# Performance work log

Measured on AMD Instinct MI355X. Metric: run time of the kernel, lower is better.

## Reference

```python
import jax, jax.numpy as jnp
import numpy as np

D_MODEL = 1024
D_FEATURE = 64
N_HEADS = D_MODEL // D_FEATURE  # 16


def setup_inputs() -> dict:
    key = jax.random.key(0)
    ks = jax.random.split(key, 11)
    B, S = 2, 2048
    s = 1.0 / np.sqrt(D_MODEL)
    inp = {
        "queries": jax.random.normal(ks[0], (B, S, D_MODEL), dtype=jnp.float32),
        "keys": jax.random.normal(ks[1], (B, S, D_MODEL), dtype=jnp.float32),
        "values": jax.random.normal(ks[2], (B, S, D_MODEL), dtype=jnp.float32),
        # Per-head Q/K/V projection weights stacked over heads: [H, d_model, d_feature]
        "Wq": jax.random.normal(ks[3], (N_HEADS, D_MODEL, D_FEATURE), dtype=jnp.float32) * s,
        "Wk": jax.random.normal(ks[4], (N_HEADS, D_MODEL, D_FEATURE), dtype=jnp.float32) * s,
        "Wv": jax.random.normal(ks[5], (N_HEADS, D_MODEL, D_FEATURE), dtype=jnp.float32) * s,
        "bq": jax.random.normal(ks[6], (N_HEADS, D_FEATURE), dtype=jnp.float32) * 0.01,
        "bk": jax.random.normal(ks[7], (N_HEADS, D_FEATURE), dtype=jnp.float32) * 0.01,
        "bv": jax.random.normal(ks[8], (N_HEADS, D_FEATURE), dtype=jnp.float32) * 0.01,
        # Output projection Linear(d_model, d_model)
        "Wo": jax.random.normal(ks[9], (D_MODEL, D_MODEL), dtype=jnp.float32) * s,
        "bo": jax.random.normal(ks[10], (D_MODEL,), dtype=jnp.float32) * 0.01,
    }
    return inp


def reference(queries, keys, values, Wq, Wk, Wv, bq, bk, bv, Wo, bo):
    # Batched equivalent of the per-head loop: all heads' Q/K/V projections
    # done as single einsums, fused multi-head scaled-dot-product attention,
    # then concat (reshape) + output projection. Dropout is identity (eval).
    scale = 1.0 / jnp.sqrt(jnp.asarray(D_FEATURE, queries.dtype))
    q = jnp.einsum("bsd,hdf->bhsf", queries, Wq) + bq[None, :, None, :]
    k = jnp.einsum("bsd,hdf->bhsf", keys, Wk) + bk[None, :, None, :]
    v = jnp.einsum("bsd,hdf->bhsf", values, Wv) + bv[None, :, None, :]
    scores = jnp.einsum("bhsf,bhtf->bhst", q, k) * scale  # [B,H,S,S]
    attn = jax.nn.softmax(scores, axis=-1)
    out = jnp.einsum("bhst,bhtf->bhsf", attn, v)  # [B,H,S,F]
    B, H, S, F = out.shape
    # torch.cat(heads, dim=2): head outputs laid out contiguously -> (h f)
    out = out.transpose(0, 2, 1, 3).reshape(B, S, H * F)
    return out @ Wo.T + bo  # final Linear(d_model, d_model)
```

## Files before the change

kernel.cpp:

```cpp
#include <hip/hip_runtime.h>
#include <hip/hip_bf16.h>

typedef __bf16 bf16_t;
typedef __bf16 bf16x4 __attribute__((ext_vector_type(4)));
typedef __bf16 bf16x8 __attribute__((ext_vector_type(8)));
typedef _Float16 f16_t;
typedef _Float16 f16x4 __attribute__((ext_vector_type(4)));
typedef _Float16 f16x8 __attribute__((ext_vector_type(8)));
typedef float f32x4 __attribute__((ext_vector_type(4)));

#define MFMA16(a, b, c)  __builtin_amdgcn_mfma_f32_16x16x32_bf16((a), (b), (c), 0, 0, 0)
#define MFMA16H(a, b, c) __builtin_amdgcn_mfma_f32_16x16x16f16((a), (b), (c), 0, 0, 0)

#define QSCALE 0.18033688089869237f

typedef __attribute__((address_space(3))) void lds_void;
typedef const __attribute__((address_space(1))) void glob_void;
static __device__ __forceinline__ void gl_lds16(const void* g, void* l) {
    __builtin_amdgcn_global_load_lds((glob_void*)g, (lds_void*)l, 16, 0, 0);
}

__global__ __launch_bounds__(256) void prep(
    const float* __restrict__ Wq, const float* __restrict__ Wk,
    const float* __restrict__ Wv, const float* __restrict__ Wo,
    const float* __restrict__ qin, const float* __restrict__ kin,
    const float* __restrict__ vin,
    bf16_t* __restrict__ WqT, bf16_t* __restrict__ WkT,
    bf16_t* __restrict__ WvT, bf16_t* __restrict__ WoT,
    bf16_t* __restrict__ qb, bf16_t* __restrict__ kb, bf16_t* __restrict__ vb)
{
    const int t = threadIdx.x;
    if (blockIdx.x < 256) {
        __shared__ float tile[64][65];
        const int h = blockIdx.x >> 4, d0 = (blockIdx.x & 15) << 6;
        const float* Ws[3] = {Wq, Wk, Wv};
        bf16_t* Wt[3] = {WqT, WkT, WvT};
        const int r = t >> 4, c4 = (t & 15) << 2;
        for (int s = 0; s < 3; ++s) {
            const float* W = Ws[s] + ((size_t)h << 16);
#pragma unroll
            for (int i = 0; i < 4; ++i) {
                float4 v = *(const float4*)&W[(size_t)(d0 + i * 16 + r) * 64 + c4];
                tile[i * 16 + r][c4 + 0] = v.x; tile[i * 16 + r][c4 + 1] = v.y;
                tile[i * 16 + r][c4 + 2] = v.z; tile[i * 16 + r][c4 + 3] = v.w;
            }
            __syncthreads();
#pragma unroll
            for (int i = 0; i < 4; ++i) {
                int f = i * 16 + r;
                bf16x4 o;
                o[0] = (bf16_t)tile[c4 + 0][f]; o[1] = (bf16_t)tile[c4 + 1][f];
                o[2] = (bf16_t)tile[c4 + 2][f]; o[3] = (bf16_t)tile[c4 + 3][f];
                *(bf16x4*)&Wt[s][(((size_t)(h << 6) + f) << 10) + d0 + c4] = o;
            }
            __syncthreads();
        }
    } else {
        size_t id = (size_t)(blockIdx.x - 256) * 256 + t;
        size_t e = id * 4;
        {
            float4 v = *(const float4*)&qin[e];
            bf16x4 o = {(bf16_t)v.x, (bf16_t)v.y, (bf16_t)v.z, (bf16_t)v.w};
            *(bf16x4*)&qb[e] = o;
        }
        {
            float4 v = *(const float4*)&kin[e];
            bf16x4 o = {(bf16_t)v.x, (bf16_t)v.y, (bf16_t)v.z, (bf16_t)v.w};
            *(bf16x4*)&kb[e] = o;
        }
        {
            float4 v = *(const float4*)&vin[e];
            bf16x4 o = {(bf16_t)v.x, (bf16_t)v.y, (bf16_t)v.z, (bf16_t)v.w};
            *(bf16x4*)&vb[e] = o;
        }
        if (id < 262144) {
            float4 v = *(const float4*)&Wo[e];
            bf16x4 o = {(bf16_t)v.x, (bf16_t)v.y, (bf16_t)v.z, (bf16_t)v.w};
            *(bf16x4*)&WoT[e] = o;
        }
    }
}

static __device__ __forceinline__ void gemm_k1024(
    const bf16_t* __restrict__ A, const bf16_t* __restrict__ B,
    int m0, int n0, bf16_t* As, bf16_t* Bs, f32x4 acc[4][4])
{
    const int tid = threadIdx.x, lane = tid & 63, w = tid >> 6;
    const int m = lane & 15, quad = lane >> 4;
    const int wm = (w >> 1) * 64, wn = (w & 1) * 64;
    const int lrow = lane >> 3, lcol = (lane & 7) * 8;

    for (int kt = 0; kt < 1024; kt += 64) {
#pragma unroll
        for (int i = 0; i < 4; ++i) {
            int chunk = i * 4 + w;
            int row = chunk * 8 + lrow;
            gl_lds16(A + (size_t)(m0 + row) * 1024 + kt + lcol, As + chunk * 512);
            gl_lds16(B + (size_t)(n0 + row) * 1024 + kt + lcol, Bs + chunk * 512);
        }
        __syncthreads();
#pragma unroll
        for (int kc = 0; kc < 2; ++kc) {
            bf16x8 af[4], bfr[4];
#pragma unroll
            for (int x = 0; x < 4; ++x) {
                af[x]  = *(const bf16x8*)&As[(wm + x * 16 + m) * 64 + kc * 32 + quad * 8];
                bfr[x] = *(const bf16x8*)&Bs[(wn + x * 16 + m) * 64 + kc * 32 + quad * 8];
            }
#pragma unroll
            for (int mt = 0; mt < 4; ++mt)
#pragma unroll
                for (int nt = 0; nt < 4; ++nt)
                    acc[mt][nt] = MFMA16(af[mt], bfr[nt], acc[mt][nt]);
        }
        __syncthreads();
    }
}

__global__ __launch_bounds__(256) void gemm_proj(
    const bf16_t* __restrict__ qb, const bf16_t* __restrict__ kb,
    const bf16_t* __restrict__ vb, const bf16_t* __restrict__ WT,
    const float* __restrict__ bq, const float* __restrict__ bk,
    const float* __restrict__ bv,
    bf16_t* __restrict__ Qs, bf16_t* __restrict__ Ksb, f16_t* __restrict__ Vt)
{
    __shared__ alignas(16) bf16_t As[8192], Bs[8192];
    const int z = blockIdx.z;
    const bf16_t* A = (z == 0) ? qb : (z == 1) ? kb : vb;
    const bf16_t* B = WT + (size_t)z * (1024 * 1024);
    const float* bias = (z == 0) ? bq : (z == 1) ? bk : bv;
    const int m0 = blockIdx.y * 128, n0 = blockIdx.x * 128;

    f32x4 zero = {0.f, 0.f, 0.f, 0.f};
    f32x4 acc[4][4];
#pragma unroll
    for (int i = 0; i < 4; ++i)
#pragma unroll
        for (int j = 0; j < 4; ++j) acc[i][j] = zero;

    gemm_k1024(A, B, m0, n0, As, Bs, acc);

    const int lane = threadIdx.x & 63, w = threadIdx.x >> 6;
    const int m = lane & 15, quad = lane >> 4;
    const int wm = (w >> 1) * 64, wn = (w & 1) * 64;

    if (z == 2) {
#pragma unroll
        for (int mt = 0; mt < 4; ++mt)
#pragma unroll
            for (int nt = 0; nt < 4; ++nt) {
                int col = n0 + wn + nt * 16 + m;
                float bb = bias[col];
                int row0 = m0 + wm + mt * 16 + quad * 4;
                int bi = row0 >> 11, s = row0 & 2047;
                f16x4 p;
#pragma unroll
                for (int r = 0; r < 4; ++r) p[r] = (f16_t)(acc[mt][nt][r] + bb);
                *(f16x4*)&Vt[((size_t)bi * 1024 + col) * 2048 + s] = p;
            }
    } else {
        bf16_t* out = z ? Ksb : Qs;
        float sc = z ? 1.0f : QSCALE;
#pragma unroll
        for (int mt = 0; mt < 4; ++mt)
#pragma unroll
            for (int nt = 0; nt < 4; ++nt) {
                int col = n0 + wn + nt * 16 + m;
                float bb = bias[col];
#pragma unroll
                for (int r = 0; r < 4; ++r) {
                    int row = m0 + wm + mt * 16 + quad * 4 + r;
                    out[(size_t)row * 1024 + col] = (bf16_t)((acc[mt][nt][r] + bb) * sc);
                }
            }
    }
}

__global__ __launch_bounds__(256) void gemm_out(
    const bf16_t* __restrict__ Aos, const bf16_t* __restrict__ WoT,
    const float* __restrict__ bo, float* __restrict__ out)
{
    __shared__ alignas(16) bf16_t As[128 * 64], Bs[64 * 64];
    const int tid = threadIdx.x, lane = tid & 63, w = tid >> 6;
    const int m = lane & 15, quad = lane >> 4;
    const int wm = (w >> 1) * 64, wn = (w & 1) * 32;
    const int m0 = blockIdx.y * 128, n0 = blockIdx.x * 64;
    const int lrow = lane >> 3, lcol = (lane & 7) * 8;

    f32x4 zero = {0.f, 0.f, 0.f, 0.f};
    f32x4 acc[4][2];
#pragma unroll
    for (int i = 0; i < 4; ++i) { acc[i][0] = zero; acc[i][1] = zero; }

    for (int kt = 0; kt < 1024; kt += 64) {
#pragma unroll
        for (int i = 0; i < 4; ++i) {
            int chunk = i * 4 + w;
            gl_lds16(Aos + (size_t)(m0 + chunk * 8 + lrow) * 1024 + kt + lcol, As + chunk * 512);
        }
#pragma unroll
        for (int i = 0; i < 2; ++i) {
            int chunk = i * 4 + w;
            gl_lds16(WoT + (size_t)(n0 + chunk * 8 + lrow) * 1024 + kt + lcol, Bs + chunk * 512);
        }
        __syncthreads();
#pragma unroll
        for (int kc = 0; kc < 2; ++kc) {
            bf16x8 af[4], bfr[2];
#pragma unroll
            for (int x = 0; x < 4; ++x)
                af[x] = *(const bf16x8*)&As[(wm + x * 16 + m) * 64 + kc * 32 + quad * 8];
#pragma unroll
            for (int x = 0; x < 2; ++x)
                bfr[x] = *(const bf16x8*)&Bs[(wn + x * 16 + m) * 64 + kc * 32 + quad * 8];
#pragma unroll
            for (int mt = 0; mt < 4; ++mt)
#pragma unroll
                for (int nt = 0; nt < 2; ++nt)
                    acc[mt][nt] = MFMA16(af[mt], bfr[nt], acc[mt][nt]);
        }
        __syncthreads();
    }

#pragma unroll
    for (int mt = 0; mt < 4; ++mt)
#pragma unroll
        for (int nt = 0; nt < 2; ++nt) {
            int col = n0 + wn + nt * 16 + m;
            float bb = bo[col];
#pragma unroll
            for (int r = 0; r < 4; ++r) {
                int row = m0 + wm + mt * 16 + quad * 4 + r;
                out[(size_t)row * 1024 + col] = acc[mt][nt][r] + bb;
            }
        }
}

__global__ __launch_bounds__(256) void attn3(
    const bf16_t* __restrict__ Qb, const bf16_t* __restrict__ Kb,
    const f16_t* __restrict__ Vt, bf16_t* __restrict__ Ob)
{
    __shared__ alignas(16) bf16_t Ks[2][32][72];
    __shared__ alignas(16) f16_t  Vts[2][64][40];

    const int tid = threadIdx.x, lane = tid & 63, w = tid >> 6;
    const int m = lane & 15, quad = lane >> 4;
    const int bh = blockIdx.y, b = bh >> 4, h = bh & 15;
    const int q0 = blockIdx.x * 128;
    const size_t base = (size_t)b * 2048 * 1024 + h * 64;
    const size_t vbase = ((size_t)b * 1024 + h * 64) * 2048;

    bf16x8 aq[2][2];
#pragma unroll
    for (int qt = 0; qt < 2; ++qt) {
        const bf16_t* qp = Qb + base + (size_t)(q0 + w * 32 + qt * 16 + m) * 1024;
        aq[qt][0] = *(const bf16x8*)(qp + quad * 8);
        aq[qt][1] = *(const bf16x8*)(qp + 32 + quad * 8);
    }
    f16x4 onesh;
#pragma unroll
    for (int j = 0; j < 4; ++j) onesh[j] = (f16_t)1.0f;

    f32x4 zero = {0.f, 0.f, 0.f, 0.f};
    f32x4 acc[2][5];
#pragma unroll
    for (int qt = 0; qt < 2; ++qt)
#pragma unroll
        for (int i = 0; i < 5; ++i) acc[qt][i] = zero;

    const int kkey = tid >> 3, kfo = (tid & 7) * 8;
    const int vf = tid >> 2, vko = (tid & 3) * 8;

    bf16x8 rk = *(const bf16x8*)(Kb + base + (size_t)kkey * 1024 + kfo);
    f16x8  rv = *(const f16x8*)(Vt + vbase + (size_t)vf * 2048 + vko);

    int buf = 0;
    for (int kt = 0; kt < 2048; kt += 32) {
        *(bf16x8*)&Ks[buf][kkey][kfo] = rk;
        *(f16x8*)&Vts[buf][vf][vko] = rv;
        __syncthreads();
        if (kt + 32 < 2048) {
            rk = *(const bf16x8*)(Kb + base + (size_t)(kt + 32 + kkey) * 1024 + kfo);
            rv = *(const f16x8*)(Vt + vbase + (size_t)vf * 2048 + kt + 32 + vko);
        }

        f32x4 s[2][2];
#pragma unroll
        for (int kl = 0; kl < 2; ++kl) {
            bf16x8 a0 = *(const bf16x8*)&Ks[buf][kl * 16 + m][quad * 8];
            bf16x8 a1 = *(const bf16x8*)&Ks[buf][kl * 16 + m][32 + quad * 8];
#pragma unroll
            for (int qt = 0; qt < 2; ++qt) {
                f32x4 t = MFMA16(a0, aq[qt][0], zero);
                s[kl][qt] = MFMA16(a1, aq[qt][1], t);
            }
        }

        f16x4 p[2][2];
#pragma unroll
        for (int qt = 0; qt < 2; ++qt)
#pragma unroll
            for (int kl = 0; kl < 2; ++kl)
#pragma unroll
                for (int r = 0; r < 4; ++r)
                    p[qt][kl][r] = (f16_t)__builtin_amdgcn_exp2f(s[kl][qt][r]);

#pragma unroll
        for (int kl = 0; kl < 2; ++kl) {
#pragma unroll
            for (int ft = 0; ft < 4; ++ft) {
                f16x4 bv = *(const f16x4*)&Vts[buf][ft * 16 + m][kl * 16 + quad * 4];
#pragma unroll
                for (int qt = 0; qt < 2; ++qt)
                    acc[qt][ft] = MFMA16H(p[qt][kl], bv, acc[qt][ft]);
            }
#pragma unroll
            for (int qt = 0; qt < 2; ++qt)
                acc[qt][4] = MFMA16H(p[qt][kl], onesh, acc[qt][4]);
        }
        buf ^= 1;
    }

#pragma unroll
    for (int qt = 0; qt < 2; ++qt)
#pragma unroll
        for (int r = 0; r < 4; ++r) {
            float inv = __builtin_amdgcn_rcpf(acc[qt][4][r]);
            int row = q0 + w * 32 + qt * 16 + quad * 4 + r;
            bf16_t* op = Ob + base + (size_t)row * 1024;
#pragma unroll
            for (int ft = 0; ft < 4; ++ft)
                op[ft * 16 + m] = (bf16_t)(acc[qt][ft][r] * inv);
        }
}

extern "C" void kernel_launch(void* const* d_in, const int* in_sizes, int n_in,
                              void* d_out, int out_size, void* d_ws, size_t ws_size,
                              hipStream_t stream)
{
    const float* queries = (const float*)d_in[0];
    const float* keys    = (const float*)d_in[1];
    const float* values  = (const float*)d_in[2];
    const float* Wq = (const float*)d_in[3];
    const float* Wk = (const float*)d_in[4];
    const float* Wv = (const float*)d_in[5];
    const float* bq = (const float*)d_in[6];
    const float* bk = (const float*)d_in[7];
    const float* bv = (const float*)d_in[8];
    const float* Wo = (const float*)d_in[9];
    const float* bo = (const float*)d_in[10];

    char* ws = (char*)d_ws;
    const size_t MB = 1024 * 1024;
    bf16_t* WqT = (bf16_t*)(ws + 0 * MB);
    bf16_t* WkT = (bf16_t*)(ws + 2 * MB);
    bf16_t* WvT = (bf16_t*)(ws + 4 * MB);
    bf16_t* WoT = (bf16_t*)(ws + 6 * MB);
    bf16_t* qb  = (bf16_t*)(ws + 8 * MB);
    bf16_t* kb  = (bf16_t*)(ws + 16 * MB);
    bf16_t* vb  = (bf16_t*)(ws + 24 * MB);
    f16_t*  Vt  = (f16_t*)(ws + 32 * MB);
    bf16_t* Qs  = (bf16_t*)d_out;
    bf16_t* Ksb = (bf16_t*)((char*)d_out + 8 * MB);
    bf16_t* Os  = qb;
    (void)WkT; (void)WvT;

    prep<<<4352, 256, 0, stream>>>(Wq, Wk, Wv, Wo, queries, keys, values,
                                   WqT, WkT, WvT, WoT, qb, kb, vb);

    gemm_proj<<<dim3(8, 32, 3), 256, 0, stream>>>(qb, kb, vb, WqT, bq, bk, bv,
                                                  Qs, Ksb, Vt);

    attn3<<<dim3(16, 32), 256, 0, stream>>>(Qs, Ksb, Vt, Os);

    gemm_out<<<dim3(16, 32), 256, 0, stream>>>(Os, WoT, bo, (float*)d_out);
}
```

Before: 240.8 us.

## Halve attention query tile to 64 rows, reorder grid, pack exp conversions

The attention kernel now gives each wave 16 query rows instead of 32, so a block covers 64 queries and the grid doubles to 1024 blocks, with batch-head as the fast grid dimension so blocks sharing K/V are scheduled together. The exp results are converted to fp16 in pairs with the packed round-toward-zero instruction. The smaller tile is meant to raise occupancy and parallelism on the many-CU GPU and to cut register pressure. In exchange, every K/V tile is loaded from global memory twice as often relative to compute, and rounding toward zero changes the probabilities slightly.

```diff
diff --git a/kernel.cpp b/kernel.cpp
--- a/kernel.cpp
+++ b/kernel.cpp
@@ -7,6 +7,7 @@
 typedef _Float16 f16_t;
 typedef _Float16 f16x4 __attribute__((ext_vector_type(4)));
 typedef _Float16 f16x8 __attribute__((ext_vector_type(8)));
+typedef __fp16 hf2 __attribute__((ext_vector_type(2)));
 typedef float f32x4 __attribute__((ext_vector_type(4)));
 
 #define MFMA16(a, b, c)  __builtin_amdgcn_mfma_f32_16x16x32_bf16((a), (b), (c), 0, 0, 0)
@@ -236,7 +237,7 @@
         }
 }
 
-__global__ __launch_bounds__(256) void attn3(
+__global__ __launch_bounds__(256) void attn4(
     const bf16_t* __restrict__ Qb, const bf16_t* __restrict__ Kb,
     const f16_t* __restrict__ Vt, bf16_t* __restrict__ Ob)
 {
@@ -245,28 +246,23 @@
 
     const int tid = threadIdx.x, lane = tid & 63, w = tid >> 6;
     const int m = lane & 15, quad = lane >> 4;
-    const int bh = blockIdx.y, b = bh >> 4, h = bh & 15;
-    const int q0 = blockIdx.x * 128;
+    const int bh = blockIdx.x, b = bh >> 4, h = bh & 15;
+    const int q0 = blockIdx.y * 64;
     const size_t base = (size_t)b * 2048 * 1024 + h * 64;
     const size_t vbase = ((size_t)b * 1024 + h * 64) * 2048;
 
-    bf16x8 aq[2][2];
-#pragma unroll
-    for (int qt = 0; qt < 2; ++qt) {
-        const bf16_t* qp = Qb + base + (size_t)(q0 + w * 32 + qt * 16 + m) * 1024;
-        aq[qt][0] = *(const bf16x8*)(qp + quad * 8);
-        aq[qt][1] = *(const bf16x8*)(qp + 32 + quad * 8);
-    }
+    const bf16_t* qp = Qb + base + (size_t)(q0 + w * 16 + m) * 1024;
+    bf16x8 aq0 = *(const bf16x8*)(qp + quad * 8);
+    bf16x8 aq1 = *(const bf16x8*)(qp + 32 + quad * 8);
+
     f16x4 onesh;
 #pragma unroll
     for (int j = 0; j < 4; ++j) onesh[j] = (f16_t)1.0f;
 
     f32x4 zero = {0.f, 0.f, 0.f, 0.f};
-    f32x4 acc[2][5];
-#pragma unroll
-    for (int qt = 0; qt < 2; ++qt)
-#pragma unroll
-        for (int i = 0; i < 5; ++i) acc[qt][i] = zero;
+    f32x4 acc[5];
+#pragma unroll
+    for (int i = 0; i < 5; ++i) acc[i] = zero;
 
     const int kkey = tid >> 3, kfo = (tid & 7) * 8;
     const int vf = tid >> 2, vko = (tid & 3) * 8;
@@ -284,54 +280,49 @@
             rv = *(const f16x8*)(Vt + vbase + (size_t)vf * 2048 + kt + 32 + vko);
         }
 
-        f32x4 s[2][2];
+        f32x4 s[2];
 #pragma unroll
         for (int kl = 0; kl < 2; ++kl) {
             bf16x8 a0 = *(const bf16x8*)&Ks[buf][kl * 16 + m][quad * 8];
             bf16x8 a1 = *(const bf16x8*)&Ks[buf][kl * 16 + m][32 + quad * 8];
-#pragma unroll
-            for (int qt = 0; qt < 2; ++qt) {
-                f32x4 t = MFMA16(a0, aq[qt][0], zero);
-                s[kl][qt] = MFMA16(a1, aq[qt][1], t);
-            }
-        }
-
-        f16x4 p[2][2];
-#pragma unroll
-        for (int qt = 0; qt < 2; ++qt)
-#pragma unroll
-            for (int kl = 0; kl < 2; ++kl)
-#pragma unroll
-                for (int r = 0; r < 4; ++r)
-                    p[qt][kl][r] = (f16_t)__builtin_amdgcn_exp2f(s[kl][qt][r]);
+            f32x4 t = MFMA16(a0, aq0, zero);
+            s[kl] = MFMA16(a1, aq1, t);
+        }
+
+        f16x4 p[2];
+#pragma unroll
+        for (int kl = 0; kl < 2; ++kl) {
+            hf2 lo = __builtin_amdgcn_cvt_pkrtz(
+                __builtin_amdgcn_exp2f(s[kl][0]),
+                __builtin_amdgcn_exp2f(s[kl][1]));
+            hf2 hi = __builtin_amdgcn_cvt_pkrtz(
+                __builtin_amdgcn_exp2f(s[kl][2]),
+                __builtin_amdgcn_exp2f(s[kl][3]));
+            p[kl][0] = lo[0]; p[kl][1] = lo[1];
+            p[kl][2] = hi[0]; p[kl][3] = hi[1];
+        }
 
 #pragma unroll
         for (int kl = 0; kl < 2; ++kl) {
 #pragma unroll
             for (int ft = 0; ft < 4; ++ft) {
                 f16x4 bv = *(const f16x4*)&Vts[buf][ft * 16 + m][kl * 16 + quad * 4];
-#pragma unroll
-                for (int qt = 0; qt < 2; ++qt)
-                    acc[qt][ft] = MFMA16H(p[qt][kl], bv, acc[qt][ft]);
-            }
-#pragma unroll
-            for (int qt = 0; qt < 2; ++qt)
-                acc[qt][4] = MFMA16H(p[qt][kl], onesh, acc[qt][4]);
+                acc[ft] = MFMA16H(p[kl], bv, acc[ft]);
+            }
+            acc[4] = MFMA16H(p[kl], onesh, acc[4]);
         }
         buf ^= 1;
     }
 
 #pragma unroll
-    for (int qt = 0; qt < 2; ++qt)
-#pragma unroll
-        for (int r = 0; r < 4; ++r) {
-            float inv = __builtin_amdgcn_rcpf(acc[qt][4][r]);
-            int row = q0 + w * 32 + qt * 16 + quad * 4 + r;
-            bf16_t* op = Ob + base + (size_t)row * 1024;
-#pragma unroll
-            for (int ft = 0; ft < 4; ++ft)
-                op[ft * 16 + m] = (bf16_t)(acc[qt][ft][r] * inv);
-        }
+    for (int r = 0; r < 4; ++r) {
+        float inv = __builtin_amdgcn_rcpf(acc[4][r]);
+        int row = q0 + w * 16 + quad * 4 + r;
+        bf16_t* op = Ob + base + (size_t)row * 1024;
+#pragma unroll
+        for (int ft = 0; ft < 4; ++ft)
+            op[ft * 16 + m] = (bf16_t)(acc[ft][r] * inv);
+    }
 }
 
 extern "C" void kernel_launch(void* const* d_in, const int* in_sizes, int n_in,
@@ -371,7 +362,7 @@
     gemm_proj<<<dim3(8, 32, 3), 256, 0, stream>>>(qb, kb, vb, WqT, bq, bk, bv,
                                                   Qs, Ksb, Vt);
 
-    attn3<<<dim3(16, 32), 256, 0, stream>>>(Qs, Ksb, Vt, Os);
+    attn4<<<dim3(32, 32), 256, 0, stream>>>(Qs, Ksb, Vt, Os);
 
     gemm_out<<<dim3(16, 32), 256, 0, stream>>>(Os, WoT, bo, (float*)d_out);
 }
```

New measurement: 250.4 us. +4.0%, slower.

## Split attention over two key halves with combine kernel and wider f16 MFMA

Applied to the files above, without the earlier changes.

The attention kernel now splits the key range into two halves along a new grid dimension. Each half writes unnormalized f16 partial outputs and fp32 row sums to workspace, and a new combine kernel adds the halves and normalizes to bf16. This doubles the number of blocks to raise CU occupancy. The P·V step also moves from 16x16x16 to 16x16x32 f16 MFMA with packed exp conversion, and launch bounds ask for 4 waves per SIMD. The cost is an extra kernel launch and extra global traffic for the partials. Storing unnormalized sums in f16 also risks overflow.

```diff
diff --git a/kernel.cpp b/kernel.cpp
--- a/kernel.cpp
+++ b/kernel.cpp
@@ -7,10 +7,11 @@
 typedef _Float16 f16_t;
 typedef _Float16 f16x4 __attribute__((ext_vector_type(4)));
 typedef _Float16 f16x8 __attribute__((ext_vector_type(8)));
+typedef __fp16 hf2 __attribute__((ext_vector_type(2)));
 typedef float f32x4 __attribute__((ext_vector_type(4)));
 
 #define MFMA16(a, b, c)  __builtin_amdgcn_mfma_f32_16x16x32_bf16((a), (b), (c), 0, 0, 0)
-#define MFMA16H(a, b, c) __builtin_amdgcn_mfma_f32_16x16x16f16((a), (b), (c), 0, 0, 0)
+#define MFMA32H(a, b, c) __builtin_amdgcn_mfma_f32_16x16x32_f16((a), (b), (c), 0, 0, 0)
 
 #define QSCALE 0.18033688089869237f
 
@@ -236,17 +237,19 @@
         }
 }
 
-__global__ __launch_bounds__(256) void attn3(
+__global__ __launch_bounds__(256, 4) void attn5(
     const bf16_t* __restrict__ Qb, const bf16_t* __restrict__ Kb,
-    const f16_t* __restrict__ Vt, bf16_t* __restrict__ Ob)
+    const f16_t* __restrict__ Vt, f16_t* __restrict__ Op, float* __restrict__ Ls)
 {
     __shared__ alignas(16) bf16_t Ks[2][32][72];
     __shared__ alignas(16) f16_t  Vts[2][64][40];
 
     const int tid = threadIdx.x, lane = tid & 63, w = tid >> 6;
     const int m = lane & 15, quad = lane >> 4;
-    const int bh = blockIdx.y, b = bh >> 4, h = bh & 15;
-    const int q0 = blockIdx.x * 128;
+    const int bh = blockIdx.x, b = bh >> 4, h = bh & 15;
+    const int q0 = blockIdx.y * 128;
+    const int ks = blockIdx.z;
+    const int kt0 = ks << 10;
     const size_t base = (size_t)b * 2048 * 1024 + h * 64;
     const size_t vbase = ((size_t)b * 1024 + h * 64) * 2048;
 
@@ -257,9 +260,9 @@
         aq[qt][0] = *(const bf16x8*)(qp + quad * 8);
         aq[qt][1] = *(const bf16x8*)(qp + 32 + quad * 8);
     }
-    f16x4 onesh;
-#pragma unroll
-    for (int j = 0; j < 4; ++j) onesh[j] = (f16_t)1.0f;
+    f16x8 ones8;
+#pragma unroll
+    for (int j = 0; j < 8; ++j) ones8[j] = (f16_t)1.0f;
 
     f32x4 zero = {0.f, 0.f, 0.f, 0.f};
     f32x4 acc[2][5];
@@ -271,15 +274,15 @@
     const int kkey = tid >> 3, kfo = (tid & 7) * 8;
     const int vf = tid >> 2, vko = (tid & 3) * 8;
 
-    bf16x8 rk = *(const bf16x8*)(Kb + base + (size_t)kkey * 1024 + kfo);
-    f16x8  rv = *(const f16x8*)(Vt + vbase + (size_t)vf * 2048 + vko);
+    bf16x8 rk = *(const bf16x8*)(Kb + base + (size_t)(kt0 + kkey) * 1024 + kfo);
+    f16x8  rv = *(const f16x8*)(Vt + vbase + (size_t)vf * 2048 + kt0 + vko);
 
     int buf = 0;
-    for (int kt = 0; kt < 2048; kt += 32) {
+    for (int kt = kt0; kt < kt0 + 1024; kt += 32) {
         *(bf16x8*)&Ks[buf][kkey][kfo] = rk;
         *(f16x8*)&Vts[buf][vf][vko] = rv;
         __syncthreads();
-        if (kt + 32 < 2048) {
+        if (kt + 32 < kt0 + 1024) {
             rk = *(const bf16x8*)(Kb + base + (size_t)(kt + 32 + kkey) * 1024 + kfo);
             rv = *(const f16x8*)(Vt + vbase + (size_t)vf * 2048 + kt + 32 + vko);
         }
@@ -296,28 +299,36 @@
             }
         }
 
-        f16x4 p[2][2];
+        f16x8 p[2];
 #pragma unroll
         for (int qt = 0; qt < 2; ++qt)
 #pragma unroll
-            for (int kl = 0; kl < 2; ++kl)
-#pragma unroll
-                for (int r = 0; r < 4; ++r)
-                    p[qt][kl][r] = (f16_t)__builtin_amdgcn_exp2f(s[kl][qt][r]);
-
-#pragma unroll
-        for (int kl = 0; kl < 2; ++kl) {
-#pragma unroll
-            for (int ft = 0; ft < 4; ++ft) {
-                f16x4 bv = *(const f16x4*)&Vts[buf][ft * 16 + m][kl * 16 + quad * 4];
-#pragma unroll
-                for (int qt = 0; qt < 2; ++qt)
-                    acc[qt][ft] = MFMA16H(p[qt][kl], bv, acc[qt][ft]);
-            }
+            for (int kl = 0; kl < 2; ++kl) {
+                hf2 lo = __builtin_amdgcn_cvt_pkrtz(
+                    __builtin_amdgcn_exp2f(s[kl][qt][0]),
+                    __builtin_amdgcn_exp2f(s[kl][qt][1]));
+                hf2 hi = __builtin_amdgcn_cvt_pkrtz(
+                    __builtin_amdgcn_exp2f(s[kl][qt][2]),
+                    __builtin_amdgcn_exp2f(s[kl][qt][3]));
+                p[qt][kl * 4 + 0] = lo[0]; p[qt][kl * 4 + 1] = lo[1];
+                p[qt][kl * 4 + 2] = hi[0]; p[qt][kl * 4 + 3] = hi[1];
+            }
+
+#pragma unroll
+        for (int ft = 0; ft < 4; ++ft) {
+            f16x4 lo = *(const f16x4*)&Vts[buf][ft * 16 + m][quad * 4];
+            f16x4 hi = *(const f16x4*)&Vts[buf][ft * 16 + m][16 + quad * 4];
+            f16x8 bv;
+#pragma unroll
+            for (int j = 0; j < 4; ++j) { bv[j] = lo[j]; bv[4 + j] = hi[j]; }
 #pragma unroll
             for (int qt = 0; qt < 2; ++qt)
-                acc[qt][4] = MFMA16H(p[qt][kl], onesh, acc[qt][4]);
-        }
+                acc[qt][ft] = MFMA32H(p[qt], bv, acc[qt][ft]);
+        }
+#pragma unroll
+        for (int qt = 0; qt < 2; ++qt)
+            acc[qt][4] = MFMA32H(p[qt], ones8, acc[qt][4]);
+
         buf ^= 1;
     }
 
@@ -325,13 +336,31 @@
     for (int qt = 0; qt < 2; ++qt)
 #pragma unroll
         for (int r = 0; r < 4; ++r) {
-            float inv = __builtin_amdgcn_rcpf(acc[qt][4][r]);
-            int row = q0 + w * 32 + qt * 16 + quad * 4 + r;
-            bf16_t* op = Ob + base + (size_t)row * 1024;
+            int grow = (b << 11) + q0 + w * 32 + qt * 16 + quad * 4 + r;
+            f16_t* op = Op + (((size_t)ks << 12) + grow) * 1024 + (h << 6);
 #pragma unroll
             for (int ft = 0; ft < 4; ++ft)
-                op[ft * 16 + m] = (bf16_t)(acc[qt][ft][r] * inv);
-        }
+                op[ft * 16 + m] = (f16_t)(acc[qt][ft][r]);
+            if (m == 0)
+                Ls[((((size_t)ks << 12) + grow) << 4) + h] = acc[qt][4][r];
+        }
+}
+
+__global__ __launch_bounds__(256) void combine(
+    const f16_t* __restrict__ Op, const float* __restrict__ Ls,
+    bf16_t* __restrict__ Os)
+{
+    size_t idx = ((size_t)blockIdx.x * 256 + threadIdx.x) * 8;
+    int row = (int)(idx >> 10), h = (int)((idx & 1023) >> 6);
+    f16x8 a = *(const f16x8*)&Op[idx];
+    f16x8 c = *(const f16x8*)&Op[(size_t)4096 * 1024 + idx];
+    float l = Ls[row * 16 + h] + Ls[4096 * 16 + row * 16 + h];
+    float inv = __builtin_amdgcn_rcpf(l);
+    bf16x8 o;
+#pragma unroll
+    for (int i = 0; i < 8; ++i)
+        o[i] = (bf16_t)(((float)a[i] + (float)c[i]) * inv);
+    *(bf16x8*)&Os[idx] = o;
 }
 
 extern "C" void kernel_launch(void* const* d_in, const int* in_sizes, int n_in,
@@ -360,6 +389,8 @@
     bf16_t* kb  = (bf16_t*)(ws + 16 * MB);
     bf16_t* vb  = (bf16_t*)(ws + 24 * MB);
     f16_t*  Vt  = (f16_t*)(ws + 32 * MB);
+    f16_t*  Op  = (f16_t*)(ws + 40 * MB);
+    float*  Lsp = (float*)(ws + 56 * MB);
     bf16_t* Qs  = (bf16_t*)d_out;
     bf16_t* Ksb = (bf16_t*)((char*)d_out + 8 * MB);
     bf16_t* Os  = qb;
@@ -371,7 +402,9 @@
     gemm_proj<<<dim3(8, 32, 3), 256, 0, stream>>>(qb, kb, vb, WqT, bq, bk, bv,
                                                   Qs, Ksb, Vt);
 
-    attn3<<<dim3(16, 32), 256, 0, stream>>>(Qs, Ksb, Vt, Os);
+    attn5<<<dim3(32, 16, 2), 256, 0, stream>>>(Qs, Ksb, Vt, Op, Lsp);
+
+    combine<<<2048, 256, 0, stream>>>(Op, Lsp, Os);
 
     gemm_out<<<dim3(16, 32), 256, 0, stream>>>(Os, WoT, bo, (float*)d_out);
 }
```

Result: faster. 234.1 us (-2.8%).
